# Performance work log

Hardware: AMD Instinct MI355X
Metric: run time of the kernel (lower is better)

## Reference

```python
import jax, jax.numpy as jnp
import numpy as np

E, H, F, T = 8, 2048, 4096, 16384  # experts, hidden, ffn, total tokens


def setup_inputs() -> dict:
    key = jax.random.key(0)
    k1, k2, k3 = jax.random.split(key, 3)
    std = 1.0 / np.sqrt(H)
    x = jax.random.normal(k1, (T, H), dtype=jnp.float32)
    # trunc_normal_(std=std) ~ normal * std for reference purposes
    w_gate_up = jax.random.normal(k2, (E, 2 * F, H), dtype=jnp.float32) * std
    w_down = jax.random.normal(k3, (E, H, F), dtype=jnp.float32) * std
    # tokens are pre-sorted by expert; uniform routing: T//E tokens per expert
    tokens_per_expert = jnp.full((E,), T // E, dtype=jnp.int64)
    return {"x": x, "w_gate_up": w_gate_up, "w_down": w_down,
            "tokens_per_expert": tokens_per_expert}


def reference(x, w_gate_up, w_down, tokens_per_expert):
    # x: [T, H] sorted by expert; uniform tokens_per_expert => grouped GEMM
    # is a batched GEMM over the expert axis (same math as the per-expert
    # sequential fallback: gate_up = xi @ w_gate_up[i].T, etc.).
    e = w_gate_up.shape[0]
    f = w_down.shape[2]
    xe = x.reshape(e, -1, x.shape[-1])                     # [E, T/E, H]
    gate_up = jnp.einsum('eth,efh->etf', xe, w_gate_up)    # [E, T/E, 2F]
    gate, up = gate_up[..., :f], gate_up[..., f:]
    hidden = jax.nn.silu(gate) * up                        # [E, T/E, F]
    out = jnp.einsum('etf,ehf->eth', hidden, w_down)       # [E, T/E, H]
    return out.reshape(x.shape)
```

## Files before the change

### kernel.cpp

```cpp
#include <hip/hip_runtime.h>
#include <stdint.h>

typedef unsigned short u16;
typedef unsigned int u32;
typedef short bf16x8 __attribute__((ext_vector_type(8)));
typedef float f32x4 __attribute__((ext_vector_type(4)));

#define E_ 8
#define H_ 2048
#define F_ 4096
#define T_ 16384
#define TE_ 2048


__device__ __forceinline__ u16 f2bf(float f) {
  u32 u = __builtin_bit_cast(u32, f);
  u32 r = (u + 0x7FFFu + ((u >> 16) & 1u)) >> 16;
  return (u16)r;
}

__device__ __forceinline__ void gload_lds16(const u16* g, u16* l) {
  __builtin_amdgcn_global_load_lds(
      (__attribute__((address_space(1))) void*)g,
      (__attribute__((address_space(3))) void*)l, 16, 0, 0);
}

__device__ __forceinline__ void mfma_b(f32x4& acc, bf16x8 a, bf16x8 b) {
  asm volatile("v_mfma_f32_16x16x32_bf16 %0, %1, %2, %0"
               : "+v"(acc)
               : "v"(a), "v"(b));
}


__global__ __launch_bounds__(256) void cvt_kernel(const float* __restrict__ src,
                                                  u16* __restrict__ dst,
                                                  long n4) {
  long i = (long)blockIdx.x * blockDim.x + threadIdx.x;
  long stride = (long)gridDim.x * blockDim.x;
  const float4* s4 = (const float4*)src;
  uint2* d4 = (uint2*)dst;
  for (; i < n4; i += stride) {
    float4 v = s4[i];
    uint2 o;
    o.x = (u32)f2bf(v.x) | ((u32)f2bf(v.y) << 16);
    o.y = (u32)f2bf(v.z) | ((u32)f2bf(v.w) << 16);
    d4[i] = o;
  }
}


__global__ __launch_bounds__(256) void gemm1_silu(const u16* __restrict__ Xb,
                                                  const u16* __restrict__ Wgu,
                                                  u16* __restrict__ Hid,
                                                  long sX, long sW, long sH) {
  const int z = blockIdx.z;
  Xb += (long)z * sX;
  Wgu += (long)z * sW;
  Hid += (long)z * sH;

  const int bx = blockIdx.x;
  const int by = blockIdx.y;
  const int tid = threadIdx.x;
  const int w = tid >> 6;
  const int lane = tid & 63;
  const int wr = w >> 1, wc = w & 1;

  __shared__ __attribute__((aligned(16))) u16 As[128 * 32];
  __shared__ __attribute__((aligned(16))) u16 Bg[64 * 32];
  __shared__ __attribute__((aligned(16))) u16 Bu[64 * 32];

  const int rowBase = by * 128;
  const int colBase = bx * 64;

  const int sr = lane >> 2;
  const int sc = (lane & 3) * 8;

  const u16* gA = Xb + (size_t)(rowBase + w * 32 + sr) * H_ + sc;
  const int bRow0 = (w & 1) * 32;
  const size_t wRow = (w < 2) ? (size_t)(colBase + bRow0 + sr) * H_
                              : (size_t)(F_ + colBase + bRow0 + sr) * H_;
  const u16* gB = Wgu + wRow + sc;
  u16* lB = (w < 2) ? (u16*)Bg : (u16*)Bu;
  const int lBoff = bRow0 * 32;

  f32x4 zero4 = {0.f, 0.f, 0.f, 0.f};
  f32x4 accG[4][2], accU[4][2];
#pragma unroll
  for (int m = 0; m < 4; ++m)
#pragma unroll
    for (int n = 0; n < 2; ++n) {
      accG[m][n] = zero4;
      accU[m][n] = zero4;
    }

  const int fr = lane & 15;
  const int fk = (lane >> 4) * 8;

  for (int k0 = 0; k0 < H_; k0 += 32) {
    gload_lds16(gA + k0, &As[(w * 32) * 32]);
    gload_lds16(gA + k0 + 16 * H_, &As[(w * 32 + 16) * 32]);
    gload_lds16(gB + k0, &lB[lBoff]);
    gload_lds16(gB + k0 + 16 * H_, &lB[lBoff + 16 * 32]);
    __syncthreads();

    bf16x8 a[4], bg[2], bu[2];
#pragma unroll
    for (int m = 0; m < 4; ++m)
      a[m] = *(const bf16x8*)&As[(wr * 64 + m * 16 + fr) * 32 + fk];
#pragma unroll
    for (int n = 0; n < 2; ++n) {
      bg[n] = *(const bf16x8*)&Bg[(wc * 32 + n * 16 + fr) * 32 + fk];
      bu[n] = *(const bf16x8*)&Bu[(wc * 32 + n * 16 + fr) * 32 + fk];
    }
#pragma unroll
    for (int m = 0; m < 4; ++m)
#pragma unroll
      for (int n = 0; n < 2; ++n) {
        mfma_b(accG[m][n], a[m], bg[n]);
        mfma_b(accU[m][n], a[m], bu[n]);
      }
    __syncthreads();
  }

  const int cr = (lane >> 4) * 4;
  const int cc = lane & 15;
#pragma unroll
  for (int m = 0; m < 4; ++m)
#pragma unroll
    for (int n = 0; n < 2; ++n)
#pragma unroll
      for (int j = 0; j < 4; ++j) {
        int row = rowBase + wr * 64 + m * 16 + cr + j;
        int col = colBase + wc * 32 + n * 16 + cc;
        float g = accG[m][n][j];
        float u = accU[m][n][j];
        float h = (g / (1.f + __expf(-g))) * u;
        Hid[(size_t)row * F_ + col] = f2bf(h);
      }
}


__global__ __launch_bounds__(256) void gemm2_down(const u16* __restrict__ Hd,
                                                  const u16* __restrict__ Wd,
                                                  float* __restrict__ Out,
                                                  long sH, long sW, long sO) {
  const int z = blockIdx.z;
  Hd += (long)z * sH;
  Wd += (long)z * sW;
  Out += (long)z * sO;

  const int bx = blockIdx.x;
  const int by = blockIdx.y;
  const int tid = threadIdx.x;
  const int w = tid >> 6;
  const int lane = tid & 63;
  const int wr = w >> 1, wc = w & 1;

  __shared__ __attribute__((aligned(16))) u16 As[128 * 32];
  __shared__ __attribute__((aligned(16))) u16 Bs[128 * 32];

  const int rowBase = by * 128;
  const int colBase = bx * 128;

  const int sr = lane >> 2;
  const int sc = (lane & 3) * 8;

  const u16* gA = Hd + (size_t)(rowBase + w * 32 + sr) * F_ + sc;
  const u16* gB = Wd + (size_t)(colBase + w * 32 + sr) * F_ + sc;

  f32x4 zero4 = {0.f, 0.f, 0.f, 0.f};
  f32x4 acc[4][4];
#pragma unroll
  for (int m = 0; m < 4; ++m)
#pragma unroll
    for (int n = 0; n < 4; ++n) acc[m][n] = zero4;

  const int fr = lane & 15;
  const int fk = (lane >> 4) * 8;

  for (int k0 = 0; k0 < F_; k0 += 32) {
    gload_lds16(gA + k0, &As[(w * 32) * 32]);
    gload_lds16(gA + k0 + 16 * F_, &As[(w * 32 + 16) * 32]);
    gload_lds16(gB + k0, &Bs[(w * 32) * 32]);
    gload_lds16(gB + k0 + 16 * F_, &Bs[(w * 32 + 16) * 32]);
    __syncthreads();

    bf16x8 a[4], b[4];
#pragma unroll
    for (int m = 0; m < 4; ++m)
      a[m] = *(const bf16x8*)&As[(wr * 64 + m * 16 + fr) * 32 + fk];
#pragma unroll
    for (int n = 0; n < 4; ++n)
      b[n] = *(const bf16x8*)&Bs[(wc * 64 + n * 16 + fr) * 32 + fk];
#pragma unroll
    for (int m = 0; m < 4; ++m)
#pragma unroll
      for (int n = 0; n < 4; ++n) mfma_b(acc[m][n], a[m], b[n]);
    __syncthreads();
  }

  const int cr = (lane >> 4) * 4;
  const int cc = lane & 15;
#pragma unroll
  for (int m = 0; m < 4; ++m)
#pragma unroll
    for (int n = 0; n < 4; ++n)
#pragma unroll
      for (int j = 0; j < 4; ++j) {
        int row = rowBase + wr * 64 + m * 16 + cr + j;
        int col = colBase + wc * 64 + n * 16 + cc;
        Out[(size_t)row * H_ + col] = acc[m][n][j];
      }
}


extern "C" void kernel_launch(void* const* d_in, const int* in_sizes, int n_in,
                              void* d_out, int out_size, void* d_ws,
                              size_t ws_size, hipStream_t stream) {
  (void)in_sizes;
  (void)n_in;
  (void)out_size;
  const float* x = (const float*)d_in[0];
  const float* wgu = (const float*)d_in[1];
  const float* wdn = (const float*)d_in[2];
  float* out = (float*)d_out;
  u16* ws = (u16*)d_ws;

  const size_t xbN = (size_t)T_ * H_;
  const size_t wguN = (size_t)E_ * 2 * F_ * H_;
  const size_t wdnN = (size_t)E_ * H_ * F_;
  const size_t hidN = (size_t)T_ * F_;
  const size_t fullBytes = (xbN + wguN + wdnN + hidN) * 2;

  dim3 blk(256);

  if (ws_size >= fullBytes) {
    u16* xb = ws;
    u16* wgub = xb + xbN;
    u16* wdnb = wgub + wguN;
    u16* hid = wdnb + wdnN;
    cvt_kernel<<<2048, blk, 0, stream>>>(x, xb, (long)(xbN / 4));
    cvt_kernel<<<4096, blk, 0, stream>>>(wgu, wgub, (long)(wguN / 4));
    cvt_kernel<<<4096, blk, 0, stream>>>(wdn, wdnb, (long)(wdnN / 4));
    gemm1_silu<<<dim3(F_ / 64, TE_ / 128, E_), blk, 0, stream>>>(
        xb, wgub, hid, (long)TE_ * H_, (long)2 * F_ * H_, (long)TE_ * F_);
    gemm2_down<<<dim3(H_ / 128, TE_ / 128, E_), blk, 0, stream>>>(
        hid, wdnb, out, (long)TE_ * F_, (long)H_ * F_, (long)TE_ * H_);
  } else {
    u16* xb = ws;
    u16* wgub = xb + (size_t)TE_ * H_;
    u16* wdnb = wgub + (size_t)2 * F_ * H_;
    u16* hid = wdnb + (size_t)H_ * F_;
    for (int e = 0; e < E_; ++e) {
      cvt_kernel<<<1024, blk, 0, stream>>>(x + (size_t)e * TE_ * H_, xb,
                                           (long)((size_t)TE_ * H_ / 4));
      cvt_kernel<<<2048, blk, 0, stream>>>(wgu + (size_t)e * 2 * F_ * H_, wgub,
                                           (long)((size_t)2 * F_ * H_ / 4));
      cvt_kernel<<<2048, blk, 0, stream>>>(wdn + (size_t)e * H_ * F_, wdnb,
                                           (long)((size_t)H_ * F_ / 4));
      gemm1_silu<<<dim3(F_ / 64, TE_ / 128, 1), blk, 0, stream>>>(xb, wgub, hid,
                                                                  0, 0, 0);
      gemm2_down<<<dim3(H_ / 128, TE_ / 128, 1), blk, 0, stream>>>(
          hid, wdnb, out + (size_t)e * TE_ * H_, 0, 0, 0);
    }
  }
}
```

Baseline: 1.301 ms.

## Triple-buffer LDS with async prefetch, XOR swizzle, and larger 512-thread GEMM tiles

Both GEMMs now use 512-thread blocks with larger output tiles (128x128 gate/up, 256x128 down) and a K-step of 64. Global-to-LDS loads go into a triple-buffered ring, and vmcnt waits let the next two stages stream in while the current one is computed, which hides memory latency that the old single-buffer load-sync-compute loop exposed. An XOR swizzle on the LDS column layout is meant to avoid bank conflicts, and s_setprio raises wave priority around the MFMA bursts. The cost is more LDS per block (144 KB) and tighter occupancy, and correctness now depends on the hand-written waitcnt counts.

```diff
diff --git a/kernel.cpp b/kernel.cpp
--- a/kernel.cpp
+++ b/kernel.cpp
@@ -12,6 +12,9 @@
 #define T_ 16384
 #define TE_ 2048
 
+#define WAITV(n) asm volatile("s_waitcnt vmcnt(" #n ")" ::: "memory")
+#define FENCE asm volatile("" ::: "memory")
+#define BAR __builtin_amdgcn_s_barrier()
 
 __device__ __forceinline__ u16 f2bf(float f) {
   u32 u = __builtin_bit_cast(u32, f);
@@ -19,7 +22,7 @@
   return (u16)r;
 }
 
-__device__ __forceinline__ void gload_lds16(const u16* g, u16* l) {
+__device__ __forceinline__ void gload16(const u16* g, u16* l) {
   __builtin_amdgcn_global_load_lds(
       (__attribute__((address_space(1))) void*)g,
       (__attribute__((address_space(3))) void*)l, 16, 0, 0);
@@ -49,7 +52,7 @@
 }
 
 
-__global__ __launch_bounds__(256) void gemm1_silu(const u16* __restrict__ Xb,
+__global__ __launch_bounds__(512) void gemm1_silu(const u16* __restrict__ Xb,
                                                   const u16* __restrict__ Wgu,
                                                   u16* __restrict__ Hid,
                                                   long sX, long sW, long sH) {
@@ -63,84 +66,103 @@
   const int tid = threadIdx.x;
   const int w = tid >> 6;
   const int lane = tid & 63;
-  const int wr = w >> 1, wc = w & 1;
-
-  __shared__ __attribute__((aligned(16))) u16 As[128 * 32];
-  __shared__ __attribute__((aligned(16))) u16 Bg[64 * 32];
-  __shared__ __attribute__((aligned(16))) u16 Bu[64 * 32];
-
-  const int rowBase = by * 128;
-  const int colBase = bx * 64;
-
-  const int sr = lane >> 2;
-  const int sc = (lane & 3) * 8;
-
-  const u16* gA = Xb + (size_t)(rowBase + w * 32 + sr) * H_ + sc;
-  const int bRow0 = (w & 1) * 32;
-  const size_t wRow = (w < 2) ? (size_t)(colBase + bRow0 + sr) * H_
-                              : (size_t)(F_ + colBase + bRow0 + sr) * H_;
-  const u16* gB = Wgu + wRow + sc;
-  u16* lB = (w < 2) ? (u16*)Bg : (u16*)Bu;
-  const int lBoff = bRow0 * 32;
-
-  f32x4 zero4 = {0.f, 0.f, 0.f, 0.f};
-  f32x4 accG[4][2], accU[4][2];
-#pragma unroll
-  for (int m = 0; m < 4; ++m)
-#pragma unroll
-    for (int n = 0; n < 2; ++n) {
-      accG[m][n] = zero4;
-      accU[m][n] = zero4;
+  const int wr = w >> 2, wc = w & 3;
+
+  __shared__ __attribute__((aligned(16))) u16 lds[3 * 24576];
+
+  const int srow = (w << 3) + (lane >> 3);
+  const int scol = (((lane & 7) ^ (lane >> 3)) << 3);
+  const u16* gA = Xb + (size_t)((by << 7) + srow) * H_ + scol;
+  const u16* gBg = Wgu + (size_t)((bx << 7) + srow) * H_ + scol;
+  const u16* gBu = gBg + (size_t)F_ * H_;
+
+  auto stage = [&](int t, int buf) {
+    u16* L = &lds[buf * 24576];
+    const int ko = t << 6;
+    const int wb = w << 3;
+#pragma unroll
+    for (int i = 0; i < 2; ++i) {
+      gload16(gA + (size_t)(i * 64) * H_ + ko, &L[((i << 6) + wb) << 6]);
+      gload16(gBg + (size_t)(i * 64) * H_ + ko,
+              &L[8192 + (((i << 6) + wb) << 6)]);
+      gload16(gBu + (size_t)(i * 64) * H_ + ko,
+              &L[16384 + (((i << 6) + wb) << 6)]);
     }
-
-  const int fr = lane & 15;
-  const int fk = (lane >> 4) * 8;
-
-  for (int k0 = 0; k0 < H_; k0 += 32) {
-    gload_lds16(gA + k0, &As[(w * 32) * 32]);
-    gload_lds16(gA + k0 + 16 * H_, &As[(w * 32 + 16) * 32]);
-    gload_lds16(gB + k0, &lB[lBoff]);
-    gload_lds16(gB + k0 + 16 * H_, &lB[lBoff + 16 * 32]);
-    __syncthreads();
-
-    bf16x8 a[4], bg[2], bu[2];
-#pragma unroll
-    for (int m = 0; m < 4; ++m)
-      a[m] = *(const bf16x8*)&As[(wr * 64 + m * 16 + fr) * 32 + fk];
-#pragma unroll
-    for (int n = 0; n < 2; ++n) {
-      bg[n] = *(const bf16x8*)&Bg[(wc * 32 + n * 16 + fr) * 32 + fk];
-      bu[n] = *(const bf16x8*)&Bu[(wc * 32 + n * 16 + fr) * 32 + fk];
-    }
-#pragma unroll
-    for (int m = 0; m < 4; ++m)
-#pragma unroll
-      for (int n = 0; n < 2; ++n) {
-        mfma_b(accG[m][n], a[m], bg[n]);
-        mfma_b(accU[m][n], a[m], bu[n]);
-      }
-    __syncthreads();
+  };
+
+  f32x4 accG[4][2] = {};
+  f32x4 accU[4][2] = {};
+  const int fr = lane & 15, q = lane >> 4, l7 = lane & 7;
+
+  auto comp = [&](int buf) {
+    const u16* L = &lds[buf * 24576];
+    bf16x8 a[4][2], bg[2][2], bu[2][2];
+#pragma unroll
+    for (int ni = 0; ni < 2; ++ni)
+#pragma unroll
+      for (int ks = 0; ks < 2; ++ks) {
+        int r = (wc << 5) + (ni << 4) + fr;
+        int off = (r << 6) + ((((ks << 2) + q) ^ l7) << 3);
+        bg[ni][ks] = *(const bf16x8*)&L[8192 + off];
+        bu[ni][ks] = *(const bf16x8*)&L[16384 + off];
+      }
+#pragma unroll
+    for (int mi = 0; mi < 4; ++mi)
+#pragma unroll
+      for (int ks = 0; ks < 2; ++ks) {
+        int r = (wr << 6) + (mi << 4) + fr;
+        a[mi][ks] = *(const bf16x8*)&L[(r << 6) + ((((ks << 2) + q) ^ l7) << 3)];
+      }
+    __builtin_amdgcn_s_setprio(1);
+#pragma unroll
+    for (int mi = 0; mi < 4; ++mi)
+#pragma unroll
+      for (int ni = 0; ni < 2; ++ni)
+#pragma unroll
+        for (int ks = 0; ks < 2; ++ks) {
+          mfma_b(accG[mi][ni], a[mi][ks], bg[ni][ks]);
+          mfma_b(accU[mi][ni], a[mi][ks], bu[ni][ks]);
+        }
+    __builtin_amdgcn_s_setprio(0);
+  };
+
+  const int NT = H_ / 64;
+  stage(0, 0);
+  stage(1, 1);
+  int b0 = 0, b1 = 1, b2 = 2;
+  for (int t = 0; t < NT - 2; ++t) {
+    stage(t + 2, b2);
+    WAITV(12);
+    BAR;
+    FENCE;
+    comp(b0);
+    FENCE;
+    BAR;
+    int tmp = b0; b0 = b1; b1 = b2; b2 = tmp;
   }
-
-  const int cr = (lane >> 4) * 4;
-  const int cc = lane & 15;
-#pragma unroll
-  for (int m = 0; m < 4; ++m)
-#pragma unroll
-    for (int n = 0; n < 2; ++n)
+  WAITV(6); BAR; FENCE;
+  comp(b0);
+  FENCE; BAR;
+  WAITV(0); BAR; FENCE;
+  comp(b1);
+
+  const int row0 = (by << 7) + (wr << 6) + (q << 2);
+  const int col0 = (bx << 7) + (wc << 5) + fr;
+#pragma unroll
+  for (int mi = 0; mi < 4; ++mi)
+#pragma unroll
+    for (int ni = 0; ni < 2; ++ni)
 #pragma unroll
       for (int j = 0; j < 4; ++j) {
-        int row = rowBase + wr * 64 + m * 16 + cr + j;
-        int col = colBase + wc * 32 + n * 16 + cc;
-        float g = accG[m][n][j];
-        float u = accU[m][n][j];
+        float g = accG[mi][ni][j];
+        float u = accU[mi][ni][j];
         float h = (g / (1.f + __expf(-g))) * u;
-        Hid[(size_t)row * F_ + col] = f2bf(h);
-      }
-}
-
-
-__global__ __launch_bounds__(256) void gemm2_down(const u16* __restrict__ Hd,
+        Hid[(size_t)(row0 + (mi << 4) + j) * F_ + col0 + (ni << 4)] = f2bf(h);
+      }
+}
+
+
+__global__ __launch_bounds__(512) void gemm2_down(const u16* __restrict__ Hd,
                                                   const u16* __restrict__ Wd,
                                                   float* __restrict__ Out,
                                                   long sH, long sW, long sO) {
@@ -156,61 +178,88 @@
   const int lane = tid & 63;
   const int wr = w >> 1, wc = w & 1;
 
-  __shared__ __attribute__((aligned(16))) u16 As[128 * 32];
-  __shared__ __attribute__((aligned(16))) u16 Bs[128 * 32];
-
-  const int rowBase = by * 128;
-  const int colBase = bx * 128;
-
-  const int sr = lane >> 2;
-  const int sc = (lane & 3) * 8;
-
-  const u16* gA = Hd + (size_t)(rowBase + w * 32 + sr) * F_ + sc;
-  const u16* gB = Wd + (size_t)(colBase + w * 32 + sr) * F_ + sc;
-
-  f32x4 zero4 = {0.f, 0.f, 0.f, 0.f};
-  f32x4 acc[4][4];
-#pragma unroll
-  for (int m = 0; m < 4; ++m)
-#pragma unroll
-    for (int n = 0; n < 4; ++n) acc[m][n] = zero4;
-
-  const int fr = lane & 15;
-  const int fk = (lane >> 4) * 8;
-
-  for (int k0 = 0; k0 < F_; k0 += 32) {
-    gload_lds16(gA + k0, &As[(w * 32) * 32]);
-    gload_lds16(gA + k0 + 16 * F_, &As[(w * 32 + 16) * 32]);
-    gload_lds16(gB + k0, &Bs[(w * 32) * 32]);
-    gload_lds16(gB + k0 + 16 * F_, &Bs[(w * 32 + 16) * 32]);
-    __syncthreads();
-
-    bf16x8 a[4], b[4];
-#pragma unroll
-    for (int m = 0; m < 4; ++m)
-      a[m] = *(const bf16x8*)&As[(wr * 64 + m * 16 + fr) * 32 + fk];
-#pragma unroll
-    for (int n = 0; n < 4; ++n)
-      b[n] = *(const bf16x8*)&Bs[(wc * 64 + n * 16 + fr) * 32 + fk];
-#pragma unroll
-    for (int m = 0; m < 4; ++m)
-#pragma unroll
-      for (int n = 0; n < 4; ++n) mfma_b(acc[m][n], a[m], b[n]);
-    __syncthreads();
+  __shared__ __attribute__((aligned(16))) u16 lds[3 * 24576];
+
+  const int srow = (w << 3) + (lane >> 3);
+  const int scol = (((lane & 7) ^ (lane >> 3)) << 3);
+  const u16* gA = Hd + (size_t)((by << 8) + srow) * F_ + scol;
+  const u16* gB = Wd + (size_t)((bx << 7) + srow) * F_ + scol;
+
+  auto stage = [&](int t, int buf) {
+    u16* L = &lds[buf * 24576];
+    const int ko = t << 6;
+    const int wb = w << 3;
+#pragma unroll
+    for (int i = 0; i < 4; ++i)
+      gload16(gA + (size_t)(i * 64) * F_ + ko, &L[((i << 6) + wb) << 6]);
+#pragma unroll
+    for (int i = 0; i < 2; ++i)
+      gload16(gB + (size_t)(i * 64) * F_ + ko,
+              &L[16384 + (((i << 6) + wb) << 6)]);
+  };
+
+  f32x4 acc[4][4] = {};
+  const int fr = lane & 15, q = lane >> 4, l7 = lane & 7;
+
+  auto comp = [&](int buf) {
+    const u16* L = &lds[buf * 24576];
+    bf16x8 a[4][2], b[4][2];
+#pragma unroll
+    for (int ni = 0; ni < 4; ++ni)
+#pragma unroll
+      for (int ks = 0; ks < 2; ++ks) {
+        int r = (wc << 6) + (ni << 4) + fr;
+        b[ni][ks] =
+            *(const bf16x8*)&L[16384 + (r << 6) + ((((ks << 2) + q) ^ l7) << 3)];
+      }
+#pragma unroll
+    for (int mi = 0; mi < 4; ++mi)
+#pragma unroll
+      for (int ks = 0; ks < 2; ++ks) {
+        int r = (wr << 6) + (mi << 4) + fr;
+        a[mi][ks] = *(const bf16x8*)&L[(r << 6) + ((((ks << 2) + q) ^ l7) << 3)];
+      }
+    __builtin_amdgcn_s_setprio(1);
+#pragma unroll
+    for (int mi = 0; mi < 4; ++mi)
+#pragma unroll
+      for (int ni = 0; ni < 4; ++ni)
+#pragma unroll
+        for (int ks = 0; ks < 2; ++ks)
+          mfma_b(acc[mi][ni], a[mi][ks], b[ni][ks]);
+    __builtin_amdgcn_s_setprio(0);
+  };
+
+  const int NT = F_ / 64;
+  stage(0, 0);
+  stage(1, 1);
+  int b0 = 0, b1 = 1, b2 = 2;
+  for (int t = 0; t < NT - 2; ++t) {
+    stage(t + 2, b2);
+    WAITV(12);
+    BAR;
+    FENCE;
+    comp(b0);
+    FENCE;
+    BAR;
+    int tmp = b0; b0 = b1; b1 = b2; b2 = tmp;
   }
-
-  const int cr = (lane >> 4) * 4;
-  const int cc = lane & 15;
-#pragma unroll
-  for (int m = 0; m < 4; ++m)
-#pragma unroll
-    for (int n = 0; n < 4; ++n)
-#pragma unroll
-      for (int j = 0; j < 4; ++j) {
-        int row = rowBase + wr * 64 + m * 16 + cr + j;
-        int col = colBase + wc * 64 + n * 16 + cc;
-        Out[(size_t)row * H_ + col] = acc[m][n][j];
-      }
+  WAITV(6); BAR; FENCE;
+  comp(b0);
+  FENCE; BAR;
+  WAITV(0); BAR; FENCE;
+  comp(b1);
+
+  const int row0 = (by << 8) + (wr << 6) + (q << 2);
+  const int col0 = (bx << 7) + (wc << 6) + fr;
+#pragma unroll
+  for (int mi = 0; mi < 4; ++mi)
+#pragma unroll
+    for (int ni = 0; ni < 4; ++ni)
+#pragma unroll
+      for (int j = 0; j < 4; ++j)
+        Out[(size_t)(row0 + (mi << 4) + j) * H_ + col0 + (ni << 4)] =
+            acc[mi][ni][j];
 }
 
 
@@ -232,19 +281,19 @@
   const size_t hidN = (size_t)T_ * F_;
   const size_t fullBytes = (xbN + wguN + wdnN + hidN) * 2;
 
-  dim3 blk(256);
+  dim3 cblk(256), gblk(512);
 
   if (ws_size >= fullBytes) {
     u16* xb = ws;
     u16* wgub = xb + xbN;
     u16* wdnb = wgub + wguN;
     u16* hid = wdnb + wdnN;
-    cvt_kernel<<<2048, blk, 0, stream>>>(x, xb, (long)(xbN / 4));
-    cvt_kernel<<<4096, blk, 0, stream>>>(wgu, wgub, (long)(wguN / 4));
-    cvt_kernel<<<4096, blk, 0, stream>>>(wdn, wdnb, (long)(wdnN / 4));
-    gemm1_silu<<<dim3(F_ / 64, TE_ / 128, E_), blk, 0, stream>>>(
+    cvt_kernel<<<2048, cblk, 0, stream>>>(x, xb, (long)(xbN / 4));
+    cvt_kernel<<<4096, cblk, 0, stream>>>(wgu, wgub, (long)(wguN / 4));
+    cvt_kernel<<<4096, cblk, 0, stream>>>(wdn, wdnb, (long)(wdnN / 4));
+    gemm1_silu<<<dim3(F_ / 128, TE_ / 128, E_), gblk, 0, stream>>>(
         xb, wgub, hid, (long)TE_ * H_, (long)2 * F_ * H_, (long)TE_ * F_);
-    gemm2_down<<<dim3(H_ / 128, TE_ / 128, E_), blk, 0, stream>>>(
+    gemm2_down<<<dim3(H_ / 128, TE_ / 256, E_), gblk, 0, stream>>>(
         hid, wdnb, out, (long)TE_ * F_, (long)H_ * F_, (long)TE_ * H_);
   } else {
     u16* xb = ws;
@@ -252,15 +301,16 @@
     u16* wdnb = wgub + (size_t)2 * F_ * H_;
     u16* hid = wdnb + (size_t)H_ * F_;
     for (int e = 0; e < E_; ++e) {
-      cvt_kernel<<<1024, blk, 0, stream>>>(x + (size_t)e * TE_ * H_, xb,
-                                           (long)((size_t)TE_ * H_ / 4));
-      cvt_kernel<<<2048, blk, 0, stream>>>(wgu + (size_t)e * 2 * F_ * H_, wgub,
-                                           (long)((size_t)2 * F_ * H_ / 4));
-      cvt_kernel<<<2048, blk, 0, stream>>>(wdn + (size_t)e * H_ * F_, wdnb,
-                                           (long)((size_t)H_ * F_ / 4));
-      gemm1_silu<<<dim3(F_ / 64, TE_ / 128, 1), blk, 0, stream>>>(xb, wgub, hid,
-                                                                  0, 0, 0);
-      gemm2_down<<<dim3(H_ / 128, TE_ / 128, 1), blk, 0, stream>>>(
+      cvt_kernel<<<1024, cblk, 0, stream>>>(x + (size_t)e * TE_ * H_, xb,
+                                            (long)((size_t)TE_ * H_ / 4));
+      cvt_kernel<<<2048, cblk, 0, stream>>>(wgu + (size_t)e * 2 * F_ * H_, wgub,
+                                            (long)((size_t)2 * F_ * H_ / 4));
+      cvt_kernel<<<2048, cblk, 0, stream>>>(wdn + (size_t)e * H_ * F_, wdnb,
+                                            (long)((size_t)H_ * F_ / 4));
+      gemm1_silu<<<dim3(F_ / 128, TE_ / 128, 1), gblk, 0, stream>>>(xb, wgub,
+                                                                    hid, 0, 0,
+                                                                    0);
+      gemm2_down<<<dim3(H_ / 128, TE_ / 256, 1), gblk, 0, stream>>>(
           hid, wdnb, out + (size_t)e * TE_ * H_, 0, 0, 0);
     }
   }
```

Measured after the change: 1.126 ms. -13.4%, faster.
